# Kernel optimization log

Measured on AMD Instinct MI355X. Metric: run time of the kernel, lower is better.

## Reference

```python
import jax, jax.numpy as jnp
import numpy as np

B, N, C_S, C_Z, C, H, PQ, PV = 1, 512, 384, 128, 16, 12, 4, 8
N_BLOCKS = 8
SCALE, EPS, INF = 10.0, 1e-8, 1e5
N_RESTYPES = 5
CAT = H * C + 4 * H * PV + H * C_Z  # IPA output concat width = 2112


def layer_norm(x, g, b):
    mu = jnp.mean(x, -1, keepdims=True)
    var = jnp.mean(jnp.square(x - mu), -1, keepdims=True)
    return (x - mu) * jax.lax.rsqrt(var + 1e-5) * g + b


def quat_mul(q, p):
    w1, x1, y1, z1 = q[..., 0], q[..., 1], q[..., 2], q[..., 3]
    w2, x2, y2, z2 = p[..., 0], p[..., 1], p[..., 2], p[..., 3]
    return jnp.stack([
        w1 * w2 - x1 * x2 - y1 * y2 - z1 * z2,
        w1 * x2 + x1 * w2 + y1 * z2 - z1 * y2,
        w1 * y2 - x1 * z2 + y1 * w2 + z1 * x2,
        w1 * z2 + x1 * y2 - y1 * x2 + z1 * w2], -1)


def quat_to_rot(q):
    w, x, y, z = q[..., 0], q[..., 1], q[..., 2], q[..., 3]
    r0 = jnp.stack([w * w + x * x - y * y - z * z, 2 * (x * y - w * z), 2 * (x * z + w * y)], -1)
    r1 = jnp.stack([2 * (x * y + w * z), w * w - x * x + y * y - z * z, 2 * (y * z - w * x)], -1)
    r2 = jnp.stack([2 * (x * z - w * y), 2 * (y * z + w * x), w * w - x * x - y * y + z * z], -1)
    return jnp.stack([r0, r1, r2], -2)  # [..., 3, 3]


def _forward(single, pair, restype, mask,
             ln_s_g, ln_s_b, ln_z_g, ln_z_b, w_in, b_in,
             wq, bq, wkv, bkv, wqp, bqp, wkvp, bkvp, wb, bb_z, head_w, wo, bo,
             ln_ipa_g, ln_ipa_b, t_w1, t_b1, t_w2, t_b2, t_w3, t_b3, ln_t_g, ln_t_b,
             w_bb, b_bb, lit_pos):
    Bv, Nv = single.shape[0], single.shape[1]
    s = layer_norm(single, ln_s_g, ln_s_b)
    z = layer_norm(pair, ln_z_g, ln_z_b)
    s = s @ w_in + b_in
    quats = jnp.zeros((Bv, Nv, 4), s.dtype).at[..., 0].set(1.0)  # identity rigid, quat fmt
    trans = jnp.zeros((Bv, Nv, 3), s.dtype)
    mask_bias = INF * (mask[..., :, None] * mask[..., None, :] - 1.0)  # [B,N,N]
    hw = jax.nn.softplus(head_w) * np.float32(np.sqrt(1.0 / (3.0 * (PQ * 9.0 / 2.0))))
    zb = jnp.transpose(z @ wb + bb_z, (0, 3, 1, 2))  # [B,H,N,N] pair bias, same each block
    lit = lit_pos[restype]  # [B,N,3atoms,3] literature backbone coords

    def run_ipa(s, rot, tr):
        q = (s @ wq + bq).reshape(Bv, Nv, H, C)
        kv = (s @ wkv + bkv).reshape(Bv, Nv, H, 2 * C)
        k, v = kv[..., :C], kv[..., C:]
        qp = (s @ wqp + bqp).reshape(Bv, Nv, 3, H * PQ).swapaxes(-1, -2)
        qp = (jnp.einsum('bnij,bnpj->bnpi', rot, qp) + tr[..., None, :]).reshape(Bv, Nv, H, PQ, 3)
        kvp = (s @ wkvp + bkvp).reshape(Bv, Nv, 3, H * (PQ + PV)).swapaxes(-1, -2)
        kvp = (jnp.einsum('bnij,bnpj->bnpi', rot, kvp) + tr[..., None, :]).reshape(Bv, Nv, H, PQ + PV, 3)
        kp, vp = kvp[..., :PQ, :], kvp[..., PQ:, :]
        a = jnp.einsum('bihc,bjhc->bhij', q, k) * np.float32(np.sqrt(1.0 / (3 * C)))
        a = a + np.float32(np.sqrt(1.0 / 3.0)) * zb
        d2 = jnp.sum(jnp.square(qp[:, :, None] - kp[:, None]), -1)  # [B,N,N,H,PQ]
        pt_att = -0.5 * jnp.sum(d2 * hw[:, None], -1)  # [B,N,N,H]
        a = jax.nn.softmax(a + jnp.transpose(pt_att, (0, 3, 1, 2)) + mask_bias[:, None], -1)
        o = jnp.einsum('bhij,bjhc->bihc', a, v).reshape(Bv, Nv, H * C)
        opt = jnp.einsum('bhij,bjhpx->bihpx', a, vp)  # attended points, global frame
        opt = jnp.einsum('bnji,bnhpj->bnhpi', rot, opt - tr[:, :, None, None, :])  # invert_apply
        opt_norm = jnp.sqrt(jnp.sum(jnp.square(opt), -1) + EPS).reshape(Bv, Nv, H * PV)
        opt_flat = jnp.moveaxis(opt.reshape(Bv, Nv, H * PV, 3), -1, -2).reshape(Bv, Nv, 3 * H * PV)
        opair = jnp.einsum('bhij,bijc->bihc', a, z).reshape(Bv, Nv, H * C_Z)
        return jnp.concatenate([o, opt_flat, opt_norm, opair], -1) @ wo + bo

    frames_l, pos_l, states_l = [], [], []
    for _ in range(N_BLOCKS):
        rot = quat_to_rot(quats)
        s = s + run_ipa(s, rot, trans)
        s = layer_norm(s, ln_ipa_g, ln_ipa_b)  # ipa dropout = identity (eval)
        t = jax.nn.relu(s @ t_w1 + t_b1)
        t = jax.nn.relu(t @ t_w2 + t_b2)
        s = layer_norm(s + t @ t_w3 + t_b3, ln_t_g, ln_t_b)  # transition (1 layer) + LN
        upd = s @ w_bb + b_bb  # [B,N,6] backbone update
        pq = jnp.concatenate([jnp.ones_like(upd[..., :1]), upd[..., :3]], -1)
        nq = quat_mul(quats, pq)
        quats = nq * jax.lax.rsqrt(jnp.sum(jnp.square(nq), -1, keepdims=True))
        trans = trans + jnp.einsum('bnij,bnj->bni', rot, upd[..., 3:])  # OLD rot applies t-update
        rot_new = quat_to_rot(quats)
        pos_l.append(jnp.einsum('bnij,bnaj->bnai', rot_new, lit) + SCALE * trans[..., None, :])
        frames_l.append(jnp.concatenate([quats, SCALE * trans], -1))
        states_l.append(s)
        quats = jax.lax.stop_gradient(quats)  # stop_rot_gradient
    return jnp.stack(frames_l), jnp.stack(pos_l), jnp.stack(states_l), s


def setup_inputs() -> dict:
    key = jax.random.key(0)
    ki = iter(jax.random.split(key, 48))
    def w(fan_in, fan_out):
        return jax.random.normal(next(ki), (fan_in, fan_out), jnp.float32) / np.sqrt(fan_in)
    inp = {
        "single": jax.random.normal(next(ki), (B, N, C_S), jnp.float32),
        "pair": jax.random.normal(next(ki), (B, N, N, C_Z), jnp.float32),
        "restype": jax.random.randint(next(ki), (B, N), 0, N_RESTYPES),
        "mask": jnp.ones((B, N), jnp.float32),
        "ln_s_g": jnp.ones((C_S,)), "ln_s_b": jnp.zeros((C_S,)),
        "ln_z_g": jnp.ones((C_Z,)), "ln_z_b": jnp.zeros((C_Z,)),
        "w_in": w(C_S, C_S), "b_in": jnp.zeros((C_S,)),
        "wq": w(C_S, H * C), "bq": jnp.zeros((H * C,)),
        "wkv": w(C_S, 2 * H * C), "bkv": jnp.zeros((2 * H * C,)),
        "wqp": w(C_S, H * PQ * 3), "bqp": jnp.zeros((H * PQ * 3,)),
        "wkvp": w(C_S, H * (PQ + PV) * 3), "bkvp": jnp.zeros((H * (PQ + PV) * 3,)),
        "wb": w(C_Z, H), "bb_z": jnp.zeros((H,)),
        "head_w": 0.1 * jax.random.normal(next(ki), (H,), jnp.float32),
        "wo": w(CAT, C_S), "bo": jnp.zeros((C_S,)),
        "ln_ipa_g": jnp.ones((C_S,)), "ln_ipa_b": jnp.zeros((C_S,)),
        "t_w1": w(C_S, C_S), "t_b1": jnp.zeros((C_S,)),
        "t_w2": w(C_S, C_S), "t_b2": jnp.zeros((C_S,)),
        "t_w3": w(C_S, C_S), "t_b3": jnp.zeros((C_S,)),
        "ln_t_g": jnp.ones((C_S,)), "ln_t_b": jnp.zeros((C_S,)),
        "w_bb": 0.001 * jax.random.normal(next(ki), (C_S, 6), jnp.float32),
        "b_bb": jnp.zeros((6,)),
        "lit_pos": jax.random.normal(next(ki), (N_RESTYPES, 3, 3), jnp.float32),
    }
    return inp


def reference(single, pair, restype, mask,
              ln_s_g, ln_s_b, ln_z_g, ln_z_b, w_in, b_in,
              wq, bq, wkv, bkv, wqp, bqp, wkvp, bkvp, wb, bb_z, head_w, wo, bo,
              ln_ipa_g, ln_ipa_b, t_w1, t_b1, t_w2, t_b2, t_w3, t_b3, ln_t_g, ln_t_b,
              w_bb, b_bb, lit_pos):
    return _forward(single, pair, restype, mask,
                    ln_s_g, ln_s_b, ln_z_g, ln_z_b, w_in, b_in,
                    wq, bq, wkv, bkv, wqp, bqp, wkvp, bkvp, wb, bb_z, head_w, wo, bo,
                    ln_ipa_g, ln_ipa_b, t_w1, t_b1, t_w2, t_b2, t_w3, t_b3, ln_t_g, ln_t_b,
                    w_bb, b_bb, lit_pos)
```

## Files before the change

### kernel.cpp

```cpp
#include <hip/hip_runtime.h>
#include <hip/hip_bf16.h>
#include <math.h>

typedef __hip_bfloat16 bf16;

#define DINL __device__ __forceinline__
DINL float b2f(bf16 x){ return __bfloat162float(x); }
DINL bf16 f2b(float x){ return __float2bfloat16(x); }

DINL float ldin(const void* p, size_t i, int isb){
    return isb ? b2f(((const bf16*)p)[i]) : ((const float*)p)[i];
}
DINL void stout(void* p, size_t i, float v, int isb){
    if(isb) ((bf16*)p)[i] = f2b(v); else ((float*)p)[i] = v;
}

static constexpr int NRES = 512;
static constexpr int CS   = 384;
static constexpr int CZ   = 128;
static constexpr int NH   = 12;
static constexpr int PQn  = 4;
static constexpr int CAT  = 2112;
static constexpr int ASTR = 516;
static constexpr int ZSTR = 136;
static constexpr int SAK  = 56;
static constexpr int KSTR = 40;

typedef __attribute__((ext_vector_type(8))) short short8;
typedef __attribute__((ext_vector_type(4))) float f32x4;

__global__ void k_detect(const void* __restrict__ mask, int* __restrict__ flag){
    if(threadIdx.x==0 && blockIdx.x==0)
        flag[0] = (((const unsigned short*)mask)[0] == 0x3F80) ? 1 : 0;
}

#define MAXSEG 32
struct ConvSegs {
    const void* src[MAXSEG];
    int dst_off[MAXSEG];
    int blk0[MAXSEG];
    int total[MAXSEG];
};

__global__ void k_conv_multi(ConvSegs sg, int nseg, float* __restrict__ wsf,
                             const int* __restrict__ dt){
    int isb = dt[0];
    int b = blockIdx.x;
    int s = 0;
    #pragma unroll 1
    while(s+1 < nseg && sg.blk0[s+1] <= b) ++s;
    int idx = (b - sg.blk0[s])*256 + threadIdx.x;
    if(idx >= sg.total[s]) return;
    wsf[(size_t)sg.dst_off[s] + idx] = ldin(sg.src[s], idx, isb);
}

#define MAXTSEG 12
struct TSegs {
    const void* src[MAXTSEG];
    size_t dst_off[MAXTSEG];
    int N[MAXTSEG];
    int dstK[MAXTSEG];
    int blk0[MAXTSEG];
    int total[MAXTSEG];
};

__global__ void k_transpose_multi(TSegs sg, int nseg, bf16* __restrict__ base,
                                  const int* __restrict__ dt){
    int isb = dt[0];
    int b = blockIdx.x;
    int s = 0;
    #pragma unroll 1
    while(s+1 < nseg && sg.blk0[s+1] <= b) ++s;
    int idx = (b - sg.blk0[s])*256 + threadIdx.x;
    if(idx >= sg.total[s]) return;
    int N = sg.N[s];
    int k = idx / N, n = idx - k*N;
    base[sg.dst_off[s] + (size_t)n*sg.dstK[s] + k] = f2b(ldin(sg.src[s], idx, isb));
}

__global__ void k_wbT(const void* __restrict__ wb, bf16* __restrict__ wbT,
                      const int* __restrict__ dt){
    int isb = dt[0];
    for(int idx=threadIdx.x; idx<16*CZ; idx+=256){
        int nn = idx>>7, kk = idx&127;
        float v = (nn < NH) ? ldin(wb, (size_t)kk*NH+nn, isb) : 0.f;
        wbT[idx] = f2b(v);
    }
}

__global__ void k_init_frames(float* __restrict__ quats, float* __restrict__ trans){
    int i = blockIdx.x*blockDim.x + threadIdx.x;
    if(i < NRES){
        quats[i*4+0]=1.f; quats[i*4+1]=0.f; quats[i*4+2]=0.f; quats[i*4+3]=0.f;
        trans[i*3+0]=0.f; trans[i*3+1]=0.f; trans[i*3+2]=0.f;
    }
}

__global__ __launch_bounds__(128) void k_ln(const void* __restrict__ in, int in_dyn,
                     float* __restrict__ out, bf16* __restrict__ out16,
                     const float* __restrict__ g, const float* __restrict__ b, int Cdim,
                     void* __restrict__ outp, size_t st_ofs, size_t fin_ofs, int mode,
                     const int* __restrict__ dt, int nsum,
                     const float* __restrict__ sbias, const float* __restrict__ sres,
                     int do_frames,
                     const float* __restrict__ wbb_f, const float* __restrict__ bbb_f,
                     const float* __restrict__ rotp, const int* __restrict__ restype,
                     const float* __restrict__ lit_f,
                     float* __restrict__ quats, float* __restrict__ trans,
                     size_t frames_ofs, size_t pos_ofs){
    int row = blockIdx.x, tid = threadIdx.x;
    int isb = dt[0];
    int isb_in = in_dyn ? isb : 0;
    float s=0.f, s2=0.f, vals[3];
    int r=0;
    for(int c=tid; c<Cdim; c+=128, ++r){
        size_t idx = (size_t)row*Cdim + c;
        float v;
        if(nsum > 0){
            const float* pf = (const float*)in;
            v = sbias[c] + sres[idx];
            for(int p=0;p<nsum;p++) v += pf[(size_t)p*NRES*Cdim + idx];
        } else {
            v = ldin(in, idx, isb_in);
        }
        vals[r]=v; s+=v; s2+=v*v;
    }
    __shared__ float red[128], red2[128];
    red[tid]=s; red2[tid]=s2; __syncthreads();
    for(int st=64; st>0; st>>=1){ if(tid<st){ red[tid]+=red[tid+st]; red2[tid]+=red2[tid+st]; } __syncthreads(); }
    float mu = red[0]/Cdim;
    float var = red2[0]/Cdim - mu*mu;
    float rs = rsqrtf(var + 1e-5f);
    float facc[6] = {};
    r=0;
    for(int c=tid; c<Cdim; c+=128, ++r){
        float v = (vals[r]-mu)*rs*g[c] + b[c];
        size_t idx = (size_t)row*Cdim + c;
        if(out)   out[idx] = v;
        if(out16) out16[idx] = f2b(v);
        if(mode >= 1){
            stout(outp, st_ofs + idx, v, isb);
            if(mode == 2) stout(outp, fin_ofs + idx, v, isb);
        }
        if(do_frames){
            #pragma unroll
            for(int j=0;j<6;j++) facc[j] += v * wbb_f[c*6+j];
        }
    }
    if(do_frames){
        int lane = tid&63, wv = tid>>6;
        #pragma unroll
        for(int m=32; m>=1; m>>=1)
            #pragma unroll
            for(int j=0;j<6;j++) facc[j] += __shfl_xor(facc[j], m, 64);
        __shared__ float fred[2][6];
        if(lane==0){
            #pragma unroll
            for(int j=0;j<6;j++) fred[wv][j] = facc[j];
        }
        __syncthreads();
        if(tid==0){
            int i = row;
            float u[6];
            #pragma unroll
            for(int j=0;j<6;j++) u[j] = fred[0][j] + fred[1][j] + bbb_f[j];
            float qw=quats[i*4], qx=quats[i*4+1], qy=quats[i*4+2], qz=quats[i*4+3];
            float nw = qw       - qx*u[0] - qy*u[1] - qz*u[2];
            float nx = qw*u[0] + qx       + qy*u[2] - qz*u[1];
            float ny = qw*u[1] - qx*u[2] + qy       + qz*u[0];
            float nz = qw*u[2] + qx*u[1] - qy*u[0] + qz;
            float rn = rsqrtf(nw*nw + nx*nx + ny*ny + nz*nz);
            nw*=rn; nx*=rn; ny*=rn; nz*=rn;
            quats[i*4]=nw; quats[i*4+1]=nx; quats[i*4+2]=ny; quats[i*4+3]=nz;
            const float* R = rotp + i*9;
            float tx = trans[i*3]   + R[0]*u[3]+R[1]*u[4]+R[2]*u[5];
            float ty = trans[i*3+1] + R[3]*u[3]+R[4]*u[4]+R[5]*u[5];
            float tz = trans[i*3+2] + R[6]*u[3]+R[7]*u[4]+R[8]*u[5];
            trans[i*3]=tx; trans[i*3+1]=ty; trans[i*3+2]=tz;
            size_t f = frames_ofs + (size_t)i*7;
            stout(outp, f+0, nw, isb); stout(outp, f+1, nx, isb);
            stout(outp, f+2, ny, isb); stout(outp, f+3, nz, isb);
            stout(outp, f+4, 10.f*tx, isb); stout(outp, f+5, 10.f*ty, isb); stout(outp, f+6, 10.f*tz, isb);
            float Rn[9];
            Rn[0]=nw*nw+nx*nx-ny*ny-nz*nz; Rn[1]=2.f*(nx*ny-nw*nz);       Rn[2]=2.f*(nx*nz+nw*ny);
            Rn[3]=2.f*(nx*ny+nw*nz);       Rn[4]=nw*nw-nx*nx+ny*ny-nz*nz; Rn[5]=2.f*(ny*nz-nw*nx);
            Rn[6]=2.f*(nx*nz-nw*ny);       Rn[7]=2.f*(ny*nz+nw*nx);       Rn[8]=nw*nw-nx*nx-ny*ny+nz*nz;
            int rt = restype[i];
            size_t po = pos_ofs + (size_t)i*9;
            #pragma unroll
            for(int a=0;a<3;a++){
                float lx=lit_f[(rt*3+a)*3+0], ly=lit_f[(rt*3+a)*3+1], lz=lit_f[(rt*3+a)*3+2];
                stout(outp, po+a*3+0, Rn[0]*lx + Rn[1]*ly + Rn[2]*lz + 10.f*tx, isb);
                stout(outp, po+a*3+1, Rn[3]*lx + Rn[4]*ly + Rn[5]*lz + 10.f*ty, isb);
                stout(outp, po+a*3+2, Rn[6]*lx + Rn[7]*ly + Rn[8]*lz + 10.f*tz, isb);
            }
        }
    }
}

__global__ __launch_bounds__(256) void k_gemm_bf(const bf16* __restrict__ A,
        const bf16* __restrict__ BT, float* __restrict__ Cf, bf16* __restrict__ C16,
        const float* __restrict__ bias, const float* __restrict__ res,
        int M, int Nn, int K, int relu, int lda){
    __shared__ bf16 As[64*SAK];
    __shared__ bf16 Bs[64*SAK];
    int tid = threadIdx.x;
    int bm = blockIdx.y*64, bn = blockIdx.x*64;
    int kofs = blockIdx.z*K;
    int wave = tid>>6, lane = tid&63;
    int quad = lane>>4, m16 = lane&15;
    int wm = (wave>>1)*32, wn = (wave&1)*32;
    int srow = wave*16 + (lane>>2);
    int scol = (lane&3)*8;
    const bf16* Ag = A  + (size_t)(bm + srow)*lda + kofs + scol;
    const bf16* Bg = BT + (size_t)(bn + srow)*lda + kofs + scol;
    int ldw = srow*SAK + scol;
    f32x4 acc[2][2] = {};
    short8 ra = *(const short8*)Ag;
    short8 rb = *(const short8*)Bg;
    int nsteps = K >> 5;
    const short* Asp = (const short*)As;
    const short* Bsp = (const short*)Bs;
    for(int s=0; s<nsteps; ++s){
        __syncthreads();
        *(short8*)(As + ldw) = ra;
        *(short8*)(Bs + ldw) = rb;
        __syncthreads();
        if(s+1 < nsteps){
            ra = *(const short8*)(Ag + (size_t)(s+1)*32);
            rb = *(const short8*)(Bg + (size_t)(s+1)*32);
        }
        short8 a0 = *(const short8*)&Asp[(wm +      m16)*SAK + quad*8];
        short8 a1 = *(const short8*)&Asp[(wm + 16 + m16)*SAK + quad*8];
        short8 b0 = *(const short8*)&Bsp[(wn +      m16)*SAK + quad*8];
        short8 b1 = *(const short8*)&Bsp[(wn + 16 + m16)*SAK + quad*8];
        acc[0][0] = __builtin_amdgcn_mfma_f32_16x16x32_bf16(a0, b0, acc[0][0], 0,0,0);
        acc[0][1] = __builtin_amdgcn_mfma_f32_16x16x32_bf16(a0, b1, acc[0][1], 0,0,0);
        acc[1][0] = __builtin_amdgcn_mfma_f32_16x16x32_bf16(a1, b0, acc[1][0], 0,0,0);
        acc[1][1] = __builtin_amdgcn_mfma_f32_16x16x32_bf16(a1, b1, acc[1][1], 0,0,0);
    }
    float* Cfz = Cf ? Cf + (size_t)blockIdx.z*M*Nn : nullptr;
    #pragma unroll
    for(int tm=0;tm<2;tm++){
        #pragma unroll
        for(int r=0;r<4;r++){
            int row = bm + wm + tm*16 + quad*4 + r;
            #pragma unroll
            for(int tn=0;tn<2;tn++){
                int col = bn + wn + tn*16 + m16;
                float v = acc[tm][tn][r];
                if(bias) v += bias[col];
                if(res)  v += res[(size_t)row*Nn + col];
                if(relu) v = fmaxf(v, 0.f);
                if(Cfz) Cfz[(size_t)row*Nn + col] = v;
                if(C16) C16[(size_t)row*Nn + col] = f2b(v);
            }
        }
    }
}

__global__ __launch_bounds__(256) void k_zb_mfma(const void* __restrict__ pair,
        const float* __restrict__ gz, const float* __restrict__ bz,
        const bf16* __restrict__ wbT, bf16* __restrict__ zb16,
        bf16* __restrict__ zn16, const int* __restrict__ dt){
    int isb = dt[0];
    __shared__ float gs[CZ], bs[CZ];
    int t = threadIdx.x;
    if(t < CZ){ gs[t]=gz[t]; bs[t]=bz[t]; }
    int wave = t>>6, lane = t&63;
    int m = lane&15, quad = lane>>4;
    int r0 = blockIdx.x*128 + wave*32;
    const short* pps = (const short*)pair;
    const float* ppf = (const float*)pair;

    short8 bfrag[4];
    const short* wbs = (const short*)wbT;
    #pragma unroll
    for(int kc=0;kc<4;kc++) bfrag[kc] = *(const short8*)(wbs + m*CZ + kc*32 + quad*8);

    float vals0[32], vals1[32];
    if(isb){
        short8 pr0[4], pr1[4];
        const short* p0 = pps + (size_t)(r0 +      m)*CZ + quad*8;
        const short* p1 = pps + (size_t)(r0 + 16 + m)*CZ + quad*8;
        #pragma unroll
        for(int kc=0;kc<4;kc++) pr0[kc] = *(const short8*)(p0 + kc*32);
        #pragma unroll
        for(int kc=0;kc<4;kc++) pr1[kc] = *(const short8*)(p1 + kc*32);
        #pragma unroll
        for(int kc=0;kc<4;kc++)
            #pragma unroll
            for(int j=0;j<8;j++){
                vals0[kc*8+j] = b2f(((const bf16*)&pr0[kc])[j]);
                vals1[kc*8+j] = b2f(((const bf16*)&pr1[kc])[j]);
            }
    } else {
        const float* p0 = ppf + (size_t)(r0 +      m)*CZ + quad*8;
        const float* p1 = ppf + (size_t)(r0 + 16 + m)*CZ + quad*8;
        #pragma unroll
        for(int kc=0;kc<4;kc++){
            *(float4*)&vals0[kc*8]   = *(const float4*)(p0 + kc*32);
            *(float4*)&vals0[kc*8+4] = *(const float4*)(p0 + kc*32 + 4);
            *(float4*)&vals1[kc*8]   = *(const float4*)(p1 + kc*32);
            *(float4*)&vals1[kc*8+4] = *(const float4*)(p1 + kc*32 + 4);
        }
    }
    __syncthreads();

    #pragma unroll
    for(int tile=0; tile<2; ++tile){
        const float* vals = tile ? vals1 : vals0;
        int rowbase = r0 + tile*16;
        int row = rowbase + m;
        float s=0.f, s2=0.f;
        #pragma unroll
        for(int j=0;j<32;j++){ float v=vals[j]; s+=v; s2+=v*v; }
        s  += __shfl_xor(s,16,64);  s  += __shfl_xor(s,32,64);
        s2 += __shfl_xor(s2,16,64); s2 += __shfl_xor(s2,32,64);
        float mu = s*(1.f/CZ);
        float var = s2*(1.f/CZ) - mu*mu;
        float rsd = rsqrtf(var + 1e-5f);
        f32x4 acc = {0.f,0.f,0.f,0.f};
        #pragma unroll
        for(int kc=0;kc<4;kc++){
            int c0 = kc*32 + quad*8;
            short8 a;
            #pragma unroll
            for(int j=0;j<8;j++){
                float zn = (vals[kc*8+j]-mu)*rsd*gs[c0+j] + bs[c0+j];
                ((bf16*)&a)[j] = f2b(zn);
            }
            *(short8*)((short*)zn16 + (size_t)row*CZ + c0) = a;
            acc = __builtin_amdgcn_mfma_f32_16x16x32_bf16(a, bfrag[kc], acc, 0, 0, 0);
        }
        if(m < NH){
            unsigned short pk[4];
            #pragma unroll
            for(int r=0;r<4;r++){ bf16 h = f2b(acc[r]); pk[r] = *(unsigned short*)&h; }
            size_t o = (size_t)m*((size_t)NRES*NRES) + (size_t)(rowbase + quad*4);
            *(uint2*)((unsigned short*)zb16 + o) = *(const uint2*)pk;
        }
    }
}


__global__ __launch_bounds__(192) void k_rotate_kv(const float* __restrict__ qpw,
        const float* __restrict__ bproj,
        const float* __restrict__ quats, const float* __restrict__ trans,
        float* __restrict__ rot,
        float* __restrict__ qp_rot, float* __restrict__ kp_rot, bf16* __restrict__ vp16,
        float* __restrict__ k_buf, bf16* __restrict__ v16, float* __restrict__ q_buf){
    int i = blockIdx.x, t = threadIdx.x;
    __shared__ float R[9], T[3];
    __shared__ float rowbuf[1152];
    const float* q0 = qpw + (size_t)i*1152;
    const float* q1 = qpw + (size_t)NRES*1152 + (size_t)i*1152;
    #pragma unroll
    for(int r=0;r<6;r++){
        int c = t + 192*r;
        rowbuf[c] = q0[c] + q1[c] + bproj[c];
    }
    if(t==0){
        float w=quats[i*4],x=quats[i*4+1],y=quats[i*4+2],z=quats[i*4+3];
        R[0]=w*w+x*x-y*y-z*z; R[1]=2.f*(x*y-w*z);     R[2]=2.f*(x*z+w*y);
        R[3]=2.f*(x*y+w*z);   R[4]=w*w-x*x+y*y-z*z;   R[5]=2.f*(y*z-w*x);
        R[6]=2.f*(x*z-w*y);   R[7]=2.f*(y*z+w*x);     R[8]=w*w-x*x-y*y+z*z;
    }
    if(t<3) T[t] = trans[i*3+t];
    __syncthreads();
    if(t<9) rot[i*9+t] = R[t];
    q_buf[(size_t)i*192 + t] = rowbuf[t];
    {
        int h = t/16, c = t%16;
        k_buf[((size_t)h*NRES + i)*16 + c] = rowbuf[192 + h*32 + c];
        v16[(size_t)i*192 + t]             = f2b(rowbuf[192 + h*32 + 16 + c]);
    }
    if(t < 48){
        float vx = rowbuf[576 + t], vy = rowbuf[576 + 48 + t], vz = rowbuf[576 + 96 + t];
        float* o = qp_rot + ((size_t)i*48 + t)*3;
        o[0] = R[0]*vx + R[1]*vy + R[2]*vz + T[0];
        o[1] = R[3]*vx + R[4]*vy + R[5]*vz + T[1];
        o[2] = R[6]*vx + R[7]*vy + R[8]*vz + T[2];
    }
    if(t < 144){
        int hp = t;
        float vx = rowbuf[720 + hp], vy = rowbuf[720 + 144 + hp], vz = rowbuf[720 + 288 + hp];
        float ox = R[0]*vx + R[1]*vy + R[2]*vz + T[0];
        float oy = R[3]*vx + R[4]*vy + R[5]*vz + T[1];
        float oz = R[6]*vx + R[7]*vy + R[8]*vz + T[2];
        int h = hp/12, p = hp%12;
        if(p < PQn){
            float* o = kp_rot + ((size_t)i*48 + h*4 + p)*3;
            o[0]=ox; o[1]=oy; o[2]=oz;
        } else {
            bf16* o = vp16 + ((size_t)i*96 + h*8 + (p-4))*3;
            o[0]=f2b(ox); o[1]=f2b(oy); o[2]=f2b(oz);
        }
    }
}

__global__ __launch_bounds__(256) void k_attn(const float* __restrict__ q_buf,
        const float* __restrict__ k_buf, const float* __restrict__ qp_rot,
        const float* __restrict__ kp_rot, const bf16* __restrict__ zb16,
        const float* __restrict__ hw_f, const float* __restrict__ bbz_f,
        const void* __restrict__ mask, bf16* __restrict__ a16,
        const int* __restrict__ dt){
    int i0 = blockIdx.x*16, h = blockIdx.y;
    int t = threadIdx.x;
    int isb = dt[0];
    __shared__ bf16 kb_s[NRES*KSTR];
    __shared__ bf16 zb_s[16*NRES];
    __shared__ bf16 as_s[16*KSTR];
    __shared__ float colc_s[NRES];
    __shared__ float mcol_s[NRES];
    __shared__ float rowc_s[16], mrow_s[16];
    __shared__ float redm[4][16], reds[4][16];
    float hwx = hw_f[h];
    float sp = (hwx > 20.f) ? hwx : log1pf(expf(hwx));
    float hw = sp * 0.13608276348795434f;
    float zbb = 0.57735026919f * bbz_f[h];
    #pragma unroll
    for(int rr=0; rr<2; ++rr){
        int j = t*2 + rr;
        const float* kr  = k_buf  + ((size_t)h*NRES + j)*16;
        const float* kpr = kp_rot + ((size_t)j*48 + h*4)*3;
        bf16* dstp = kb_s + j*KSTR;
        float kv[16], pv[12];
        *(float4*)&kv[0]  = *(const float4*)(kr);
        *(float4*)&kv[4]  = *(const float4*)(kr + 4);
        *(float4*)&kv[8]  = *(const float4*)(kr + 8);
        *(float4*)&kv[12] = *(const float4*)(kr + 12);
        *(float4*)&pv[0]  = *(const float4*)(kpr);
        *(float4*)&pv[4]  = *(const float4*)(kpr + 4);
        *(float4*)&pv[8]  = *(const float4*)(kpr + 8);
        #pragma unroll
        for(int c=0;c<16;c++) dstp[c] = f2b(kv[c]);
        float s2k = 0.f;
        #pragma unroll
        for(int p=0;p<12;p++){ float v = pv[p]; s2k += v*v; dstp[16+p] = f2b(v); }
        dstp[28]=f2b(0.f); dstp[29]=f2b(0.f); dstp[30]=f2b(0.f); dstp[31]=f2b(0.f);
        colc_s[j] = -0.5f*hw*s2k;
        mcol_s[j] = ldin(mask, j, isb);
    }
    {
        const short8* zsrc = (const short8*)((const unsigned short*)zb16 + (size_t)h*NRES*NRES + (size_t)i0*NRES);
        short8* zdst = (short8*)zb_s;
        #pragma unroll
        for(int r=0;r<4;r++) zdst[t + r*256] = zsrc[t + r*256];
    }
    if(t < 16){
        int m = t;
        const float* qr = q_buf + (size_t)(i0+m)*192 + h*16;
        bf16* dstp = as_s + m*KSTR;
        float qv[16], qpv[12];
        *(float4*)&qv[0]  = *(const float4*)(qr);
        *(float4*)&qv[4]  = *(const float4*)(qr + 4);
        *(float4*)&qv[8]  = *(const float4*)(qr + 8);
        *(float4*)&qv[12] = *(const float4*)(qr + 12);
        const float* qpr = qp_rot + ((size_t)(i0+m)*48 + h*4)*3;
        *(float4*)&qpv[0] = *(const float4*)(qpr);
        *(float4*)&qpv[4] = *(const float4*)(qpr + 4);
        *(float4*)&qpv[8] = *(const float4*)(qpr + 8);
        #pragma unroll
        for(int c=0;c<16;c++) dstp[c] = f2b(qv[c]*0.14433756729740643f);
        float s2q = 0.f;
        #pragma unroll
        for(int p=0;p<12;p++){ float v = qpv[p]; s2q += v*v; dstp[16+p] = f2b(v*hw); }
        dstp[28]=f2b(0.f); dstp[29]=f2b(0.f); dstp[30]=f2b(0.f); dstp[31]=f2b(0.f);
        rowc_s[m] = -0.5f*hw*s2q;
        mrow_s[m] = ldin(mask, i0+m, isb);
    }
    __syncthreads();
    int lane = t&63, wv = t>>6;
    int quad = lane>>4, m16 = lane&15;
    short8 afrag = *(const short8*)((const short*)as_s + m16*KSTR + quad*8);
    float l[8][4];
    #pragma unroll
    for(int tt=0; tt<8; ++tt){
        int jt = wv*8 + tt;
        short8 bfrag = *(const short8*)((const short*)kb_s + (jt*16+m16)*KSTR + quad*8);
        f32x4 acc = {0.f,0.f,0.f,0.f};
        acc = __builtin_amdgcn_mfma_f32_16x16x32_bf16(afrag, bfrag, acc, 0,0,0);
        int j = jt*16 + m16;
        float cc = colc_s[j] + zbb;
        float mj = mcol_s[j];
        #pragma unroll
        for(int r=0;r<4;r++){
            int row = quad*4 + r;
            float zbv = b2f(zb_s[row*NRES + j]);
            l[tt][r] = acc[r] + 0.57735026919f*zbv + cc + rowc_s[row]
                     + 100000.0f*(mrow_s[row]*mj - 1.0f);
        }
    }
    float lm[4], ls[4];
    #pragma unroll
    for(int r=0;r<4;r++){
        float m = l[0][r];
        #pragma unroll
        for(int tt=1;tt<8;tt++) m = fmaxf(m, l[tt][r]);
        #pragma unroll
        for(int msk=1; msk<16; msk<<=1) m = fmaxf(m, __shfl_xor(m, msk, 64));
        lm[r] = m;
        float s = 0.f;
        #pragma unroll
        for(int tt=0;tt<8;tt++){ float e = expf(l[tt][r]-m); l[tt][r] = e; s += e; }
        #pragma unroll
        for(int msk=1; msk<16; msk<<=1) s += __shfl_xor(s, msk, 64);
        ls[r] = s;
    }
    if(m16 == 0){
        #pragma unroll
        for(int r=0;r<4;r++){ redm[wv][quad*4+r] = lm[r]; reds[wv][quad*4+r] = ls[r]; }
    }
    __syncthreads();
    #pragma unroll
    for(int r=0;r<4;r++){
        int row = quad*4+r;
        float M = redm[0][row];
        #pragma unroll
        for(int w=1;w<4;w++) M = fmaxf(M, redm[w][row]);
        float S = 0.f;
        #pragma unroll
        for(int w=0;w<4;w++) S += reds[w][row]*expf(redm[w][row]-M);
        float f = expf(lm[r]-M)/S;
        #pragma unroll
        for(int tt=0;tt<8;tt++){
            int j = (wv*8+tt)*16 + m16;
            a16[((size_t)h*NRES + i0+row)*NRES + j] = f2b(l[tt][r]*f);
        }
    }
}

__global__ __launch_bounds__(512) void k_attn_out(const bf16* __restrict__ a16,
        const bf16* __restrict__ v16, const bf16* __restrict__ vp16,
        const bf16* __restrict__ zn16,
        const float* __restrict__ rot, const float* __restrict__ trans,
        bf16* __restrict__ o_cat16){
    int i = blockIdx.x, t = threadIdx.x;
    __shared__ float a_sf[NH*ASTR];
    __shared__ bf16  zn_s[32*ZSTR];
    __shared__ float opt_s[288];
    for(int idx=t; idx<NH*NRES; idx+=512){
        int h = idx>>9, j = idx&511;
        a_sf[h*ASTR + j] = b2f(a16[((size_t)h*NRES + i)*NRES + j]);
    }
    int lane = t&63, quad = lane>>4, m16 = lane&15;
    int wv = t>>6;
    int jj = t>>4, c8 = (t&15)*8;
    int pc = t;
    int h0 = (pc<192) ? (pc>>4) : (pc-192)/24;
    const bf16* s0 = (pc<192) ? (v16 + pc) : (vp16 + (pc-192));
    int st0 = (pc<192) ? 192 : 288;
    const bf16* s1 = vp16 + 192 + t;
    int h1 = (192 + t)/24;
    float acc0 = 0.f, acc1 = 0.f;
    f32x4 macc[4] = {};
    __syncthreads();
    for(int j0=0; j0<NRES; j0+=32){
        if(j0) __syncthreads();
        {
            size_t pb = ((size_t)i*NRES + j0+jj)*CZ + c8;
            short8 z8 = *(const short8*)((const short*)zn16 + pb);
            *(short8*)&zn_s[jj*ZSTR + c8] = z8;
        }
        __syncthreads();
        if(wv < 6){
            const float* ap0 = a_sf + h0*ASTR;
            #pragma unroll
            for(int u=0; u<32; u+=4){
                int j = j0+u;
                float4 a4 = *(const float4*)(ap0 + j);
                acc0 += a4.x*b2f(s0[(size_t)j*st0])     + a4.y*b2f(s0[(size_t)(j+1)*st0])
                      + a4.z*b2f(s0[(size_t)(j+2)*st0]) + a4.w*b2f(s0[(size_t)(j+3)*st0]);
            }
            if(t < 96){
                const float* ap1 = a_sf + h1*ASTR;
                #pragma unroll
                for(int u=0; u<32; u+=4){
                    int j = j0+u;
                    float4 a4 = *(const float4*)(ap1 + j);
                    acc1 += a4.x*b2f(s1[(size_t)j*288])     + a4.y*b2f(s1[(size_t)(j+1)*288])
                          + a4.z*b2f(s1[(size_t)(j+2)*288]) + a4.w*b2f(s1[(size_t)(j+3)*288]);
                }
            }
        } else {
            float4 af0 = *(const float4*)&a_sf[m16*ASTR + j0 + quad*8];
            float4 af1 = *(const float4*)&a_sf[m16*ASTR + j0 + quad*8 + 4];
            short8 afrag;
            float az[8] = {af0.x,af0.y,af0.z,af0.w,af1.x,af1.y,af1.z,af1.w};
            #pragma unroll
            for(int r=0;r<8;r++) ((bf16*)&afrag)[r] = f2b((m16 < NH) ? az[r] : 0.f);
            int cbase = (wv-6)*64;
            #pragma unroll
            for(int tn=0; tn<4; ++tn){
                int c0 = cbase + tn*16;
                short8 bfrag;
                #pragma unroll
                for(int r=0;r<8;r++) ((bf16*)&bfrag)[r] = zn_s[(quad*8+r)*ZSTR + c0 + m16];
                macc[tn] = __builtin_amdgcn_mfma_f32_16x16x32_bf16(afrag, bfrag, macc[tn], 0,0,0);
            }
        }
    }
    if(wv >= 6){
        int cbase = (wv-6)*64;
        #pragma unroll
        for(int tn=0; tn<4; ++tn){
            int c = cbase + tn*16 + m16;
            #pragma unroll
            for(int r=0;r<4;r++){
                int h = quad*4 + r;
                if(h < NH) o_cat16[(size_t)i*CAT + 576 + h*CZ + c] = f2b(macc[tn][r]);
            }
        }
    } else {
        if(pc < 192) o_cat16[(size_t)i*CAT + pc] = f2b(acc0);
        else         opt_s[pc-192] = acc0;
        if(t < 96)   opt_s[192+t] = acc1;
    }
    __syncthreads();
    if(t < 96){
        float R0=rot[i*9+0],R1=rot[i*9+1],R2=rot[i*9+2];
        float R3=rot[i*9+3],R4=rot[i*9+4],R5=rot[i*9+5];
        float R6=rot[i*9+6],R7=rot[i*9+7],R8=rot[i*9+8];
        float T0=trans[i*3+0],T1=trans[i*3+1],T2=trans[i*3+2];
        const float* v = opt_s + t*3;
        float vx=v[0]-T0, vy=v[1]-T1, vz=v[2]-T2;
        float ox = R0*vx + R3*vy + R6*vz;
        float oy = R1*vx + R4*vy + R7*vz;
        float oz = R2*vx + R5*vy + R8*vz;
        bf16* o = o_cat16 + (size_t)i*CAT;
        o[192 +       t] = f2b(ox);
        o[192 +  96 + t] = f2b(oy);
        o[192 + 192 + t] = f2b(oz);
        o[480 + t] = f2b(sqrtf(ox*ox + oy*oy + oz*oz + 1e-8f));
    }
}


extern "C" void kernel_launch(void* const* d_in, const int* in_sizes, int n_in,
                              void* d_out, int out_size, void* d_ws, size_t ws_size,
                              hipStream_t stream){
    (void)in_sizes; (void)n_in; (void)out_size; (void)ws_size;
    const void* single = d_in[0];
    const void* pair   = d_in[1];
    const int*  restype= (const int*)d_in[2];
    const void* mask   = d_in[3];

    float* wsf = (float*)d_ws;
    bf16*  wsb = (bf16*)d_ws;
    size_t off = 0;
    auto alloc  = [&](size_t n){ float* p = wsf + off; off += (n + 3) & ~(size_t)3; return p; };
    auto allocB = [&](size_t n){ bf16* p = (bf16*)(wsf + off); off += ((n+1)/2 + 3) & ~(size_t)3; return p; };
    int*   dflag  = (int*)alloc(4);
    float* s      = alloc((size_t)NRES*CS);
    float* stmp   = alloc((size_t)NRES*CS);
    float* pw     = alloc((size_t)3*NRES*CS);
    float* qpw    = alloc((size_t)2*NRES*1152);
    float* q_buf  = alloc((size_t)NRES*192);
    float* qp_rot = alloc((size_t)NRES*144);
    float* kp_rot = alloc((size_t)NRES*144);
    float* k_bufp = alloc((size_t)NH*NRES*16);
    float* quats  = alloc(NRES*4);
    float* trans  = alloc(NRES*3);
    float* rot    = alloc(NRES*9);
    bf16*  a16    = allocB((size_t)NH*NRES*NRES);
    bf16*  zb16   = allocB((size_t)NH*NRES*NRES);
    bf16*  zn16   = allocB((size_t)NRES*NRES*CZ);
    bf16*  v16    = allocB((size_t)NRES*192);
    bf16*  vp16   = allocB((size_t)NRES*288);
    bf16*  o_cat16= allocB((size_t)NRES*CAT);
    bf16*  sin16  = allocB((size_t)NRES*CS);
    bf16*  s16    = allocB((size_t)NRES*CS);
    bf16*  t116   = allocB((size_t)NRES*CS);
    bf16*  t216   = allocB((size_t)NRES*CS);
    bf16*  WprojT = allocB((size_t)1152*CS);
    bf16*  w_inT  = allocB((size_t)CS*CS);
    bf16*  woT    = allocB((size_t)CS*CAT);
    bf16*  tw1T   = allocB((size_t)CS*CS);
    bf16*  tw2T   = allocB((size_t)CS*CS);
    bf16*  tw3T   = allocB((size_t)CS*CS);
    bf16*  wbT    = allocB(16*CZ);
    float* b_in_f = alloc(CS);
    float* bproj  = alloc(1152);
    float* bo_f   = alloc(CS);
    float* tb1f   = alloc(CS);
    float* tb2f   = alloc(CS);
    float* tb3f   = alloc(CS);
    float* lnsg   = alloc(CS);
    float* lnsb   = alloc(CS);
    float* lnig   = alloc(CS);
    float* lnib   = alloc(CS);
    float* lntg   = alloc(CS);
    float* lntb   = alloc(CS);
    float* gz_f   = alloc(CZ);
    float* bz_f   = alloc(CZ);
    float* bbz_f  = alloc(16);
    float* hw_f   = alloc(16);
    float* wbb_f  = alloc(CS*6);
    float* bbb_f  = alloc(8);
    float* lit_f  = alloc(48);

    const size_t OF_FRAMES = 0;
    const size_t OF_POS    = 28672;
    const size_t OF_STATES = 65536;
    const size_t OF_FINAL  = 1638400;

    auto cdiv = [](int a, int b){ return (a+b-1)/b; };

    k_detect<<<1,64,0,stream>>>(mask, dflag);

    ConvSegs sg;
    int nseg = 0, blk = 0;
    auto plain = [&](const void* src, float* dst, int total){
        sg.src[nseg]=src; sg.dst_off[nseg]=(int)(dst - wsf);
        sg.total[nseg]=total; sg.blk0[nseg]=blk;
        blk += (total+255)/256; ++nseg;
    };
    plain(d_in[11], bproj,     192);
    plain(d_in[13], bproj+192, 384);
    plain(d_in[15], bproj+576, 144);
    plain(d_in[17], bproj+720, 432);
    plain(d_in[9],  b_in_f, CS);
    plain(d_in[22], bo_f,   CS);
    plain(d_in[26], tb1f,   CS);
    plain(d_in[28], tb2f,   CS);
    plain(d_in[30], tb3f,   CS);
    plain(d_in[4],  lnsg,   CS);
    plain(d_in[5],  lnsb,   CS);
    plain(d_in[23], lnig,   CS);
    plain(d_in[24], lnib,   CS);
    plain(d_in[31], lntg,   CS);
    plain(d_in[32], lntb,   CS);
    plain(d_in[6],  gz_f,   CZ);
    plain(d_in[7],  bz_f,   CZ);
    plain(d_in[19], bbz_f,  NH);
    plain(d_in[20], hw_f,   NH);
    plain(d_in[34], bbb_f,  6);
    plain(d_in[35], lit_f,  45);
    plain(d_in[33], wbb_f,  CS*6);
    k_conv_multi<<<blk,256,0,stream>>>(sg, nseg, wsf, dflag);

    TSegs tg;
    int ntseg = 0, tblk = 0;
    auto trs = [&](const void* src, int K, int N, bf16* dst, int rowofs, int dstK){
        tg.src[ntseg]=src;
        tg.dst_off[ntseg]=(size_t)(dst - wsb) + (size_t)rowofs*dstK;
        tg.N[ntseg]=N; tg.dstK[ntseg]=dstK;
        tg.total[ntseg]=K*N; tg.blk0[ntseg]=tblk;
        tblk += (K*N+255)/256; ++ntseg;
    };
    trs(d_in[10], CS, 192, WprojT, 0,   CS);
    trs(d_in[12], CS, 384, WprojT, 192, CS);
    trs(d_in[14], CS, 144, WprojT, 576, CS);
    trs(d_in[16], CS, 432, WprojT, 720, CS);
    trs(d_in[8],  CS, CS,  w_inT,  0,   CS);
    trs(d_in[21], CAT, CS, woT,    0,   CAT);
    trs(d_in[25], CS, CS,  tw1T,   0,   CS);
    trs(d_in[27], CS, CS,  tw2T,   0,   CS);
    trs(d_in[29], CS, CS,  tw3T,   0,   CS);
    k_transpose_multi<<<tblk,256,0,stream>>>(tg, ntseg, wsb, dflag);
    k_wbT<<<1,256,0,stream>>>(d_in[18], wbT, dflag);

    k_zb_mfma<<<NRES*NRES/128,256,0,stream>>>(pair, gz_f, bz_f, wbT, zb16, zn16, dflag);

    k_ln<<<NRES,128,0,stream>>>(single, 1, nullptr, sin16, lnsg, lnsb, CS, nullptr, 0, 0, 0,
                                dflag, 0, nullptr, nullptr,
                                0, nullptr, nullptr, nullptr, nullptr, nullptr,
                                nullptr, nullptr, 0, 0);
    {
        dim3 g(CS/64, NRES/64);
        k_gemm_bf<<<g,256,0,stream>>>(sin16, w_inT, s, s16, b_in_f, nullptr, NRES, CS, CS, 0, CS);
    }
    k_init_frames<<<cdiv(NRES,256),256,0,stream>>>(quats, trans);

    for(int bi=0; bi<8; ++bi){
        {
            dim3 gp(1152/64, NRES/64, 2);
            k_gemm_bf<<<gp,256,0,stream>>>(s16, WprojT, qpw, nullptr, nullptr, nullptr,
                                           NRES, 1152, 192, 0, CS);
        }
        k_rotate_kv<<<NRES,192,0,stream>>>(qpw, bproj, quats, trans, rot, qp_rot, kp_rot,
                                           vp16, k_bufp, v16, q_buf);
        {
            dim3 g(NRES/16, NH);
            k_attn<<<g,256,0,stream>>>(q_buf, k_bufp, qp_rot, kp_rot, zb16, hw_f, bbz_f, mask, a16, dflag);
        }
        k_attn_out<<<NRES,512,0,stream>>>(a16, v16, vp16, zn16, rot, trans, o_cat16);
        {
            dim3 gw(CS/64, NRES/64, 3);
            k_gemm_bf<<<gw,256,0,stream>>>(o_cat16, woT, pw, nullptr, nullptr, nullptr,
                                           NRES, CS, 704, 0, CAT);
            k_ln<<<NRES,128,0,stream>>>(pw, 0, s, s16, lnig, lnib, CS, nullptr, 0, 0, 0,
                                        dflag, 3, bo_f, s,
                                        0, nullptr, nullptr, nullptr, nullptr, nullptr,
                                        nullptr, nullptr, 0, 0);
            dim3 g(CS/64, NRES/64);
            k_gemm_bf<<<g,256,0,stream>>>(s16,  tw1T, nullptr, t116, tb1f, nullptr, NRES, CS, CS, 1, CS);
            k_gemm_bf<<<g,256,0,stream>>>(t116, tw2T, nullptr, t216, tb2f, nullptr, NRES, CS, CS, 1, CS);
            dim3 g3(CS/64, NRES/64, 2);
            k_gemm_bf<<<g3,256,0,stream>>>(t216, tw3T, pw, nullptr, nullptr, nullptr,
                                           NRES, CS, 192, 0, CS);
            k_ln<<<NRES,128,0,stream>>>(pw, 0, s, s16, lntg, lntb, CS, d_out,
                                        OF_STATES + (size_t)bi*NRES*CS, OF_FINAL,
                                        (bi==7) ? 2 : 1, dflag, 2, tb3f, s,
                                        1, wbb_f, bbb_f, rot, restype, lit_f,
                                        quats, trans,
                                        OF_FRAMES + (size_t)bi*NRES*7,
                                        OF_POS + (size_t)bi*NRES*9);
        }
    }
}
```

Measured before the change: 1.389 ms.

## Fuse residual LN, transition MLP, LN and frame update into one kernel

```diff
diff --git a/kernel.cpp b/kernel.cpp
--- a/kernel.cpp
+++ b/kernel.cpp
@@ -25,6 +25,7 @@
 static constexpr int ZSTR = 136;
 static constexpr int SAK  = 56;
 static constexpr int KSTR = 40;
+static constexpr int XSTR = 392;
 
 typedef __attribute__((ext_vector_type(8))) short short8;
 typedef __attribute__((ext_vector_type(4))) float f32x4;
@@ -99,15 +100,7 @@
 __global__ __launch_bounds__(128) void k_ln(const void* __restrict__ in, int in_dyn,
                      float* __restrict__ out, bf16* __restrict__ out16,
                      const float* __restrict__ g, const float* __restrict__ b, int Cdim,
-                     void* __restrict__ outp, size_t st_ofs, size_t fin_ofs, int mode,
-                     const int* __restrict__ dt, int nsum,
-                     const float* __restrict__ sbias, const float* __restrict__ sres,
-                     int do_frames,
-                     const float* __restrict__ wbb_f, const float* __restrict__ bbb_f,
-                     const float* __restrict__ rotp, const int* __restrict__ restype,
-                     const float* __restrict__ lit_f,
-                     float* __restrict__ quats, float* __restrict__ trans,
-                     size_t frames_ofs, size_t pos_ofs){
+                     const int* __restrict__ dt){
     int row = blockIdx.x, tid = threadIdx.x;
     int isb = dt[0];
     int isb_in = in_dyn ? isb : 0;
@@ -115,14 +108,7 @@
     int r=0;
     for(int c=tid; c<Cdim; c+=128, ++r){
         size_t idx = (size_t)row*Cdim + c;
-        float v;
-        if(nsum > 0){
-            const float* pf = (const float*)in;
-            v = sbias[c] + sres[idx];
-            for(int p=0;p<nsum;p++) v += pf[(size_t)p*NRES*Cdim + idx];
-        } else {
-            v = ldin(in, idx, isb_in);
-        }
+        float v = ldin(in, idx, isb_in);
         vals[r]=v; s+=v; s2+=v*v;
     }
     __shared__ float red[128], red2[128];
@@ -131,39 +117,142 @@
     float mu = red[0]/Cdim;
     float var = red2[0]/Cdim - mu*mu;
     float rs = rsqrtf(var + 1e-5f);
-    float facc[6] = {};
     r=0;
     for(int c=tid; c<Cdim; c+=128, ++r){
         float v = (vals[r]-mu)*rs*g[c] + b[c];
         size_t idx = (size_t)row*Cdim + c;
         if(out)   out[idx] = v;
         if(out16) out16[idx] = f2b(v);
-        if(mode >= 1){
-            stout(outp, st_ofs + idx, v, isb);
-            if(mode == 2) stout(outp, fin_ofs + idx, v, isb);
-        }
-        if(do_frames){
-            #pragma unroll
-            for(int j=0;j<6;j++) facc[j] += v * wbb_f[c*6+j];
-        }
-    }
-    if(do_frames){
-        int lane = tid&63, wv = tid>>6;
-        #pragma unroll
-        for(int m=32; m>=1; m>>=1)
+    }
+}
+
+__global__ __launch_bounds__(256) void k_mlp(
+        const float* __restrict__ pw, const float* __restrict__ bo_f,
+        float* __restrict__ s, bf16* __restrict__ s16,
+        const float* __restrict__ lnig, const float* __restrict__ lnib,
+        const bf16* __restrict__ tw1T, const float* __restrict__ tb1f,
+        const bf16* __restrict__ tw2T, const float* __restrict__ tb2f,
+        const bf16* __restrict__ tw3T, const float* __restrict__ tb3f,
+        const float* __restrict__ lntg, const float* __restrict__ lntb,
+        void* __restrict__ outp, size_t st_ofs, size_t fin_ofs, int mode,
+        const int* __restrict__ dt,
+        const float* __restrict__ wbb_f, const float* __restrict__ bbb_f,
+        const float* __restrict__ rotp, const int* __restrict__ restype,
+        const float* __restrict__ lit_f,
+        float* __restrict__ quats, float* __restrict__ trans,
+        size_t frames_ofs, size_t pos_ofs){
+    __shared__ float sip[16*CS];
+    __shared__ bf16  xa[16*XSTR];
+    int t = threadIdx.x;
+    int w = t>>6, lane = t&63;
+    int quad = lane>>4, m16 = lane&15;
+    int b0 = blockIdx.x*16;
+    int isb = dt[0];
+
+    for(int rr=0; rr<4; ++rr){
+        int r = w*4+rr, gr = b0+r;
+        float v[6];
+        float sum=0.f, sq=0.f;
+        #pragma unroll
+        for(int kk=0;kk<6;kk++){
+            int c = lane + kk*64;
+            size_t idx = (size_t)gr*CS + c;
+            float x = bo_f[c] + s[idx] + pw[idx]
+                    + pw[(size_t)NRES*CS + idx] + pw[2*(size_t)NRES*CS + idx];
+            v[kk]=x; sum+=x; sq+=x*x;
+        }
+        #pragma unroll
+        for(int m=32;m>=1;m>>=1){ sum+=__shfl_xor(sum,m,64); sq+=__shfl_xor(sq,m,64); }
+        float mu = sum*(1.f/CS);
+        float rs = rsqrtf(sq*(1.f/CS) - mu*mu + 1e-5f);
+        #pragma unroll
+        for(int kk=0;kk<6;kk++){
+            int c = lane + kk*64;
+            float x = (v[kk]-mu)*rs*lnig[c] + lnib[c];
+            sip[r*CS+c] = x;
+            xa[r*XSTR+c] = f2b(x);
+        }
+    }
+    __syncthreads();
+
+    #pragma unroll
+    for(int L=0; L<3; ++L){
+        const bf16* WT   = (L==0) ? tw1T : (L==1) ? tw2T : tw3T;
+        const float* bias= (L==0) ? tb1f : (L==1) ? tb2f : tb3f;
+        f32x4 acc[6] = {};
+        for(int k=0;k<12;k++){
+            short8 a = *(const short8*)((const short*)xa + m16*XSTR + k*32 + quad*8);
+            short8 bfr[6];
+            #pragma unroll
+            for(int nt=0;nt<6;nt++){
+                int n0 = (w*6+nt)*16;
+                bfr[nt] = *(const short8*)((const short*)WT + (size_t)(n0+m16)*CS + k*32 + quad*8);
+            }
+            #pragma unroll
+            for(int nt=0;nt<6;nt++)
+                acc[nt] = __builtin_amdgcn_mfma_f32_16x16x32_bf16(a, bfr[nt], acc[nt], 0,0,0);
+        }
+        __syncthreads();
+        if(L<2){
+            #pragma unroll
+            for(int nt=0;nt<6;nt++){
+                int col = (w*6+nt)*16 + m16;
+                float bb = bias[col];
+                #pragma unroll
+                for(int r=0;r<4;r++){
+                    int row = quad*4+r;
+                    xa[row*XSTR+col] = f2b(fmaxf(acc[nt][r] + bb, 0.f));
+                }
+            }
+        } else {
+            #pragma unroll
+            for(int nt=0;nt<6;nt++){
+                int col = (w*6+nt)*16 + m16;
+                float bb = bias[col];
+                #pragma unroll
+                for(int r=0;r<4;r++){
+                    int row = quad*4+r;
+                    sip[row*CS+col] += acc[nt][r] + bb;
+                }
+            }
+        }
+        __syncthreads();
+    }
+
+    for(int rr=0; rr<4; ++rr){
+        int r = w*4+rr, gr = b0+r;
+        float v[6], facc[6]={};
+        float sum=0.f, sq=0.f;
+        #pragma unroll
+        for(int kk=0;kk<6;kk++){
+            float x = sip[r*CS + lane + kk*64];
+            v[kk]=x; sum+=x; sq+=x*x;
+        }
+        #pragma unroll
+        for(int m=32;m>=1;m>>=1){ sum+=__shfl_xor(sum,m,64); sq+=__shfl_xor(sq,m,64); }
+        float mu = sum*(1.f/CS);
+        float rs = rsqrtf(sq*(1.f/CS) - mu*mu + 1e-5f);
+        #pragma unroll
+        for(int kk=0;kk<6;kk++){
+            int c = lane + kk*64;
+            size_t idx = (size_t)gr*CS + c;
+            float x = (v[kk]-mu)*rs*lntg[c] + lntb[c];
+            s[idx] = x; s16[idx] = f2b(x);
+            stout(outp, st_ofs + idx, x, isb);
+            if(mode == 2) stout(outp, fin_ofs + idx, x, isb);
+            #pragma unroll
+            for(int j=0;j<6;j++) facc[j] += x * wbb_f[c*6+j];
+        }
+        #pragma unroll
+        for(int m=32;m>=1;m>>=1){
             #pragma unroll
             for(int j=0;j<6;j++) facc[j] += __shfl_xor(facc[j], m, 64);
-        __shared__ float fred[2][6];
+        }
         if(lane==0){
-            #pragma unroll
-            for(int j=0;j<6;j++) fred[wv][j] = facc[j];
-        }
-        __syncthreads();
-        if(tid==0){
-            int i = row;
+            int i = gr;
             float u[6];
             #pragma unroll
-            for(int j=0;j<6;j++) u[j] = fred[0][j] + fred[1][j] + bbb_f[j];
+            for(int j=0;j<6;j++) u[j] = facc[j] + bbb_f[j];
             float qw=quats[i*4], qx=quats[i*4+1], qy=quats[i*4+2], qz=quats[i*4+3];
             float nw = qw       - qx*u[0] - qy*u[1] - qz*u[2];
             float nx = qw*u[0] + qx       + qy*u[2] - qz*u[1];
@@ -763,10 +852,7 @@
 
     k_zb_mfma<<<NRES*NRES/128,256,0,stream>>>(pair, gz_f, bz_f, wbT, zb16, zn16, dflag);
 
-    k_ln<<<NRES,128,0,stream>>>(single, 1, nullptr, sin16, lnsg, lnsb, CS, nullptr, 0, 0, 0,
-                                dflag, 0, nullptr, nullptr,
-                                0, nullptr, nullptr, nullptr, nullptr, nullptr,
-                                nullptr, nullptr, 0, 0);
+    k_ln<<<NRES,128,0,stream>>>(single, 1, nullptr, sin16, lnsg, lnsb, CS, dflag);
     {
         dim3 g(CS/64, NRES/64);
         k_gemm_bf<<<g,256,0,stream>>>(sin16, w_inT, s, s16, b_in_f, nullptr, NRES, CS, CS, 0, CS);
@@ -790,23 +876,15 @@
             dim3 gw(CS/64, NRES/64, 3);
             k_gemm_bf<<<gw,256,0,stream>>>(o_cat16, woT, pw, nullptr, nullptr, nullptr,
                                            NRES, CS, 704, 0, CAT);
-            k_ln<<<NRES,128,0,stream>>>(pw, 0, s, s16, lnig, lnib, CS, nullptr, 0, 0, 0,
-                                        dflag, 3, bo_f, s,
-                                        0, nullptr, nullptr, nullptr, nullptr, nullptr,
-                                        nullptr, nullptr, 0, 0);
-            dim3 g(CS/64, NRES/64);
-            k_gemm_bf<<<g,256,0,stream>>>(s16,  tw1T, nullptr, t116, tb1f, nullptr, NRES, CS, CS, 1, CS);
-            k_gemm_bf<<<g,256,0,stream>>>(t116, tw2T, nullptr, t216, tb2f, nullptr, NRES, CS, CS, 1, CS);
-            dim3 g3(CS/64, NRES/64, 2);
-            k_gemm_bf<<<g3,256,0,stream>>>(t216, tw3T, pw, nullptr, nullptr, nullptr,
-                                           NRES, CS, 192, 0, CS);
-            k_ln<<<NRES,128,0,stream>>>(pw, 0, s, s16, lntg, lntb, CS, d_out,
-                                        OF_STATES + (size_t)bi*NRES*CS, OF_FINAL,
-                                        (bi==7) ? 2 : 1, dflag, 2, tb3f, s,
-                                        1, wbb_f, bbb_f, rot, restype, lit_f,
-                                        quats, trans,
-                                        OF_FRAMES + (size_t)bi*NRES*7,
-                                        OF_POS + (size_t)bi*NRES*9);
-        }
-    }
-}
+            k_mlp<<<NRES/16,256,0,stream>>>(pw, bo_f, s, s16, lnig, lnib,
+                                            tw1T, tb1f, tw2T, tb2f, tw3T, tb3f,
+                                            lntg, lntb,
+                                            d_out, OF_STATES + (size_t)bi*NRES*CS, OF_FINAL,
+                                            (bi==7) ? 2 : 1, dflag,
+                                            wbb_f, bbb_f, rot, restype, lit_f,
+                                            quats, trans,
+                                            OF_FRAMES + (size_t)bi*NRES*7,
+                                            OF_POS + (size_t)bi*NRES*9);
+        }
+    }
+}
```

Measured after the change: 1.508 ms. 1.09x slower.
